# Kernel tuning notes

Hardware: AMD Instinct MI355X
Metric: run time of the kernel (lower is better)

## Reference

```python
import jax, jax.numpy as jnp
import numpy as np

B, T, D = 2, 2048, 1024
H, HD = 16, 64
MAX_LEN = 2048


def setup_inputs() -> dict:
    key = jax.random.key(0)
    ks = jax.random.split(key, 7)
    s = 0.02
    return {
        "x": jax.random.normal(ks[0], (B, T, D), dtype=jnp.float32),
        "qkv_w": jax.random.normal(ks[1], (3 * D, D), dtype=jnp.float32) * s,
        "qkv_b": jax.random.normal(ks[2], (3 * D,), dtype=jnp.float32) * s,
        "out_w": jax.random.normal(ks[3], (D, D), dtype=jnp.float32) * s,
        "out_b": jax.random.normal(ks[4], (D,), dtype=jnp.float32) * s,
        "rel_pos": jax.random.normal(ks[5], (2 * MAX_LEN - 1, HD), dtype=jnp.float32),
        "rpe_w": jax.random.normal(ks[6], (HD,), dtype=jnp.float32) * s,
    }


def reference(x, qkv_w, qkv_b, out_w, out_b, rel_pos, rpe_w):
    Bq, Tq, Dq = x.shape
    scale = HD ** -0.5
    qkv = x @ qkv_w.T + qkv_b  # [B,T,3D]
    qkv = qkv.reshape(Bq, Tq, 3, H, HD)
    q = qkv[:, :, 0].transpose(0, 2, 1, 3)  # [B,H,T,HD]
    k = qkv[:, :, 1].transpose(0, 2, 1, 3)
    v = qkv[:, :, 2].transpose(0, 2, 1, 3)
    scores = jnp.einsum('bhqd,bhkd->bhqk', q, k) * scale  # [B,H,T,T]
    # relative position bias: gather rel embeddings, project to scalar
    rel_idx = jnp.arange(Tq)[None, :] - jnp.arange(Tq)[:, None] + MAX_LEN - 1  # [T,T]
    bias = (rel_pos @ rpe_w)[rel_idx]  # project first (cheap), then gather -> [T,T]
    scores = scores + bias[None, None]
    attn = jax.nn.softmax(scores, axis=-1)
    out = jnp.einsum('bhqk,bhkd->bhqd', attn, v)  # [B,H,T,HD]
    out = out.transpose(0, 2, 1, 3).reshape(Bq, Tq, Dq)
    return out @ out_w.T + out_b
```

## Files before the change

kernel.cpp:

```cpp
#include <hip/hip_runtime.h>
#include <math.h>

#define B_ 2
#define T_ 2048
#define D_ 1024
#define H_ 16
#define HD_ 64
#define MAXLEN_ 2048
#define N3D_ 3072
#define M_ (B_ * T_)
#define KA 1024

#define SCALE_L2E 0.18033688011116215f
#define L2E 1.4426950408889634f

typedef unsigned short ushort_t;
typedef __attribute__((ext_vector_type(8))) short short8;
typedef __attribute__((ext_vector_type(4))) float floatx4;
#define MFMA16(a, b, c) __builtin_amdgcn_mfma_f32_16x16x32_bf16(a, b, c, 0, 0, 0)

static __device__ __forceinline__ ushort_t f2bf(float f) {
    unsigned u = __float_as_uint(f);
    unsigned r = (u + 0x7FFFu + ((u >> 16) & 1u)) >> 16;
    return (ushort_t)r;
}
static __device__ __forceinline__ unsigned packrnu(float a, float b) {
    unsigned ua = __float_as_uint(a) + 0x8000u;
    unsigned ub = __float_as_uint(b) + 0x8000u;
    return __builtin_amdgcn_perm(ub, ua, 0x07060302u);
}

static __device__ __forceinline__ void gld16(const ushort_t* g, ushort_t* l) {
    __builtin_amdgcn_global_load_lds(
        (const __attribute__((address_space(1))) void*)g,
        (__attribute__((address_space(3))) void*)l, 16, 0, 0);
}

__global__ __launch_bounds__(256) void cvt_all(
    const float* __restrict__ x, const float* __restrict__ qw,
    const float* __restrict__ ow, const float* __restrict__ rel_pos,
    const float* __restrict__ rpe_w,
    ushort_t* __restrict__ Xc, ushort_t* __restrict__ QWc,
    ushort_t* __restrict__ OWc, float* __restrict__ biasp)
{
    const int row = blockIdx.x;
    if (row < M_ + N3D_ + D_) {
        const float* src; ushort_t* dst; int r;
        if (row < M_)            { src = x;  dst = Xc;  r = row; }
        else if (row < M_ + N3D_){ src = qw; dst = QWc; r = row - M_; }
        else                     { src = ow; dst = OWc; r = row - M_ - N3D_; }
        const int c = threadIdx.x * 4;
        float4 v = *(const float4*)(src + (size_t)r * 1024 + c);
        ushort4 hv;
        hv.x = f2bf(v.x); hv.y = f2bf(v.y); hv.z = f2bf(v.z); hv.w = f2bf(v.w);
        *(ushort4*)(dst + (size_t)r * KA + c) = hv;
    } else {
        const int wv = threadIdx.x >> 6, lane = threadIdx.x & 63;
        const int r = (row - (M_ + N3D_ + D_)) * 4 + wv;
        if (r < 2 * MAXLEN_ - 1) {
            float v = rel_pos[(size_t)r * HD_ + lane] * rpe_w[lane];
#pragma unroll
            for (int off = 32; off; off >>= 1) v += __shfl_down(v, off);
            if (lane == 0) biasp[r] = v * L2E;
        }
    }
}

__global__ __launch_bounds__(512, 2) void qkv_mfma(
    const ushort_t* __restrict__ Ac, const ushort_t* __restrict__ Bc,
    const float* __restrict__ bias,
    ushort_t* __restrict__ Qs, ushort_t* __restrict__ Khi,
    ushort_t* __restrict__ Vt)
{
    __shared__ __align__(16) ushort_t LDS[2][2][32 * 512];

    const int tid = threadIdx.x;
    const int wv = tid >> 6, lane = tid & 63;
    const int l16 = lane & 15, quad = lane >> 4;
    const int wr = wv >> 2, wc = wv & 3;

    const int orig = blockIdx.y * 12 + blockIdx.x;
    const int swz = (orig & 7) * 24 + (orig >> 3);
    const int m0 = (swz / 12) * 256, n0 = (swz % 12) * 256;

    floatx4 acc[8][4];
#pragma unroll
    for (int i = 0; i < 8; ++i)
#pragma unroll
        for (int j = 0; j < 4; ++j) acc[i][j] = (floatx4){0.f, 0.f, 0.f, 0.f};

    short8 af[4][2];
    short8 bf[2][2][2];

#define BARX() asm volatile("s_barrier" ::: "memory")
#define WAITVM(n) asm volatile("s_waitcnt vmcnt(" #n ")" ::: "memory")

#define STAGE(bufi, ab, unit, tile) do {                                      \
    const ushort_t* _src = (ab) ? Bc : Ac;                                    \
    const int _rc = (ab) ? n0 : m0;                                           \
    const int _I = (unit) * 8 + wv;                                           \
    const ushort_t* _g = _src + (size_t)(_rc + _I * 16 + l16) * KA            \
                              + ((tile) * 64 + quad * 8);                     \
    ushort_t* _l = &LDS[bufi][ab][(_I * 2) * 512];                            \
    gld16(_g, _l);                                                            \
    gld16(_g + 32, _l + 512);                                                 \
} while (0)

#define RD_AF(bufi, mi) do {                                                  \
    _Pragma("unroll") for (int ii = 0; ii < 4; ++ii) {                        \
        const int _I = wr * 8 + (mi) * 4 + ii;                                \
        af[ii][0] = *(const short8*)(&LDS[bufi][0][(_I * 2 + 0) * 512] + lane * 8); \
        af[ii][1] = *(const short8*)(&LDS[bufi][0][(_I * 2 + 1) * 512] + lane * 8); \
    } } while (0)

#define RD_BF(bufi, ni) do {                                                  \
    _Pragma("unroll") for (int jj = 0; jj < 2; ++jj) {                        \
        const int _I = wc * 4 + (ni) * 2 + jj;                                \
        bf[ni][jj][0] = *(const short8*)(&LDS[bufi][1][(_I * 2 + 0) * 512] + lane * 8); \
        bf[ni][jj][1] = *(const short8*)(&LDS[bufi][1][(_I * 2 + 1) * 512] + lane * 8); \
    } } while (0)

#define MM(mi, ni) do {                                                       \
    __builtin_amdgcn_s_setprio(1);                                            \
    _Pragma("unroll") for (int ii = 0; ii < 4; ++ii)                          \
    _Pragma("unroll") for (int jj = 0; jj < 2; ++jj) {                        \
        acc[(mi)*4+ii][(ni)*2+jj] = MFMA16(af[ii][0], bf[ni][jj][0], acc[(mi)*4+ii][(ni)*2+jj]); \
        acc[(mi)*4+ii][(ni)*2+jj] = MFMA16(af[ii][1], bf[ni][jj][1], acc[(mi)*4+ii][(ni)*2+jj]); \
    }                                                                         \
    __builtin_amdgcn_s_setprio(0);                                            \
} while (0)

    STAGE(0, 1, 0, 0); STAGE(0, 1, 1, 0);
    STAGE(0, 0, 0, 0); STAGE(0, 0, 1, 0);
    STAGE(1, 1, 0, 1); STAGE(1, 1, 1, 1);
    WAITVM(4);
    BARX();

#pragma unroll 1
    for (int j = 0; j < 8; ++j) {
        const int tY  = 2 * j + 1;
        const int tX2 = (2 * j + 2) & 15;
        const int tY2 = (2 * j + 3) & 15;
        RD_AF(0, 0); RD_BF(0, 0); STAGE(1, 0, 0, tY);  BARX(); MM(0, 0); BARX();
        RD_BF(0, 1);              STAGE(1, 0, 1, tY);  BARX(); MM(0, 1); BARX();
        RD_AF(0, 1);              STAGE(0, 1, 0, tX2); BARX(); MM(1, 0); BARX();
                                  STAGE(0, 1, 1, tX2); BARX(); MM(1, 1);
        WAITVM(4); BARX();
        RD_AF(1, 0); RD_BF(1, 0); STAGE(0, 0, 0, tX2); BARX(); MM(0, 0); BARX();
        RD_BF(1, 1);              STAGE(0, 0, 1, tX2); BARX(); MM(0, 1); BARX();
        RD_AF(1, 1);              STAGE(1, 1, 0, tY2); BARX(); MM(1, 0); BARX();
                                  STAGE(1, 1, 1, tY2); BARX(); MM(1, 1);
        WAITVM(4); BARX();
    }

#undef BARX
#undef WAITVM
#undef STAGE
#undef RD_AF
#undef RD_BF
#undef MM

#pragma unroll
    for (int mi = 0; mi < 8; ++mi) {
#pragma unroll
        for (int r = 0; r < 4; ++r) {
            const int m = m0 + wr * 128 + mi * 16 + quad * 4 + r;
            const int bb = m >> 11, t = m & 2047;
#pragma unroll
            for (int jj = 0; jj < 4; ++jj) {
                const int n = n0 + wc * 64 + jj * 16 + l16;
                const int c = n >> 10, h = (n >> 6) & 15, hd = n & 63;
                const float v = acc[mi][jj][r] + bias[n];
                const size_t idx = (((size_t)bb * H_ + h) * T_ + t) * HD_ + hd;
                if (c == 0) { Qs[idx] = f2bf(v * SCALE_L2E); }
                else if (c == 1) { Khi[idx] = f2bf(v); }
                else { Vt[(((size_t)bb * H_ + h) * HD_ + hd) * T_ + t] = f2bf(v); }
            }
        }
    }
}

__global__ __launch_bounds__(256) void out_mfma(
    const ushort_t* __restrict__ Ac, const ushort_t* __restrict__ Bc,
    const float* __restrict__ bias, float* __restrict__ Out)
{
    __shared__ __align__(16) ushort_t As[2][16 * 512];
    __shared__ __align__(16) ushort_t Bs[2][8 * 512];
    const int tid = threadIdx.x;
    const int wv = tid >> 6, lane = tid & 63;
    const int l16 = lane & 15, quad = lane >> 4;
    const int wm = wv & 1, wn = wv >> 1;

    const int orig = blockIdx.y * 16 + blockIdx.x;
    const int swz = (orig & 7) * 64 + (orig >> 3);
    const int m0 = (swz >> 4) * 128, n0 = (swz & 15) * 64;

    floatx4 acc[4][2];
#pragma unroll
    for (int i = 0; i < 4; ++i)
#pragma unroll
        for (int j = 0; j < 2; ++j) acc[i][j] = (floatx4){0.f, 0.f, 0.f, 0.f};

    auto stage = [&](int bufi, int kk) {
#pragma unroll
        for (int c = 0; c < 4; ++c) {
            const int b = wv * 4 + c;
            const int i = b >> 1, ks = b & 1;
            const int k = kk + ks * 32 + quad * 8;
            gld16(Ac + (size_t)(m0 + i * 16 + l16) * KA + k, As[bufi] + b * 512);
        }
#pragma unroll
        for (int c = 0; c < 2; ++c) {
            const int b = wv * 2 + c;
            const int j = b >> 1, ks = b & 1;
            const int k = kk + ks * 32 + quad * 8;
            gld16(Bc + (size_t)(n0 + j * 16 + l16) * KA + k, Bs[bufi] + b * 512);
        }
    };

    stage(0, 0);
    __syncthreads();

#pragma unroll 1
    for (int t = 0; t < 16; ++t) {
        const int cur = t & 1;
        if (t < 15) stage(cur ^ 1, (t + 1) * 64);
#pragma unroll
        for (int ks = 0; ks < 2; ++ks) {
            short8 af[4], bf[2];
#pragma unroll
            for (int ii = 0; ii < 4; ++ii)
                af[ii] = *(const short8*)(As[cur] + ((wm * 4 + ii) * 2 + ks) * 512 + lane * 8);
#pragma unroll
            for (int jj = 0; jj < 2; ++jj)
                bf[jj] = *(const short8*)(Bs[cur] + ((wn * 2 + jj) * 2 + ks) * 512 + lane * 8);
#pragma unroll
            for (int ii = 0; ii < 4; ++ii)
#pragma unroll
                for (int jj = 0; jj < 2; ++jj)
                    acc[ii][jj] = MFMA16(af[ii], bf[jj], acc[ii][jj]);
        }
        if (t < 15) __syncthreads();
    }

#pragma unroll
    for (int ii = 0; ii < 4; ++ii) {
#pragma unroll
        for (int r = 0; r < 4; ++r) {
            const int m = m0 + wm * 64 + ii * 16 + quad * 4 + r;
#pragma unroll
            for (int jj = 0; jj < 2; ++jj) {
                const int n = n0 + wn * 32 + jj * 16 + l16;
                Out[(size_t)m * D_ + n] = acc[ii][jj][r] + bias[n];
            }
        }
    }
}

__global__ __launch_bounds__(256) void attn_mfma(
    const ushort_t* __restrict__ Qs, const ushort_t* __restrict__ Khi,
    const ushort_t* __restrict__ Vt, const float* __restrict__ biasp,
    ushort_t* __restrict__ AOc)
{
    __shared__ __align__(16) ushort_t KS[2][8 * 512];
    __shared__ __align__(16) ushort_t VS[2][8 * 512];
    __shared__ __align__(16) ushort_t PS[4][2][1024];

    const int i = blockIdx.x;
    const int j = i >> 3;
    const int bh = (i & 7) + 8 * (j >> 4);
    const int q0 = (j & 15) * 128;
    const int tid = threadIdx.x;
    const int wv = tid >> 6, lane = tid & 63;
    const int l16 = lane & 15, quad = lane >> 4;

    const int qw = q0 + wv * 32;

    short8 qh[2][2];
#pragma unroll
    for (int u = 0; u < 2; ++u) {
        const size_t qoff = ((size_t)bh * T_ + qw + u * 16 + l16) * HD_ + quad * 8;
        qh[u][0] = *(const short8*)(Qs + qoff);
        qh[u][1] = *(const short8*)(Qs + qoff + 32);
    }

    float l_r[2] = {0.f, 0.f};
    floatx4 o_acc[4][2];
#pragma unroll
    for (int g2 = 0; g2 < 4; ++g2)
#pragma unroll
        for (int u = 0; u < 2; ++u) o_acc[g2][u] = (floatx4){0.f, 0.f, 0.f, 0.f};

    const ushort_t* gK = Khi + (size_t)bh * T_ * HD_;
    const ushort_t* gV = Vt + (size_t)bh * HD_ * T_;
    const int c0base = 2047 + quad * 4 - (qw + 16 + l16);
    const int qdbase = quad >> 1;

    const size_t kstage = (size_t)(wv * 16 + l16) * HD_ + quad * 8;
    const size_t vstage = (size_t)(wv * 16 + l16) * T_ + quad * 8;

    gld16(gK + kstage,      KS[0] + (wv * 2 + 0) * 512);
    gld16(gK + kstage + 32, KS[0] + (wv * 2 + 1) * 512);
    gld16(gV + vstage,      VS[0] + (wv * 2 + 0) * 512);
    gld16(gV + vstage + 32, VS[0] + (wv * 2 + 1) * 512);
    __syncthreads();

    for (int t = 0; t < 32; ++t) {
        const int k0 = t * 64;
        const int buf = t & 1, nbuf = buf ^ 1;

        float4 f4[5];
        {
            const float* bp = biasp + (c0base + k0);
#pragma unroll
            for (int z = 0; z < 5; ++z)
                __builtin_memcpy(&f4[z], bp + z * 16, 16);
        }

        if (t < 31) {
            const size_t koff = kstage + (size_t)(k0 + 64) * HD_;
            gld16(gK + koff,      KS[nbuf] + (wv * 2 + 0) * 512);
            gld16(gK + koff + 32, KS[nbuf] + (wv * 2 + 1) * 512);
            const size_t voff = vstage + (size_t)(k0 + 64);
            gld16(gV + voff,      VS[nbuf] + (wv * 2 + 0) * 512);
            gld16(gV + voff + 32, VS[nbuf] + (wv * 2 + 1) * 512);
        }

#pragma unroll
        for (int g = 0; g < 4; ++g) {
            const short8 kh0 = *(const short8*)(KS[buf] + (g * 2 + 0) * 512 + lane * 8);
            const short8 kh1 = *(const short8*)(KS[buf] + (g * 2 + 1) * 512 + lane * 8);
            const int qd = 2 * (g & 1) + qdbase;
#pragma unroll
            for (int u = 0; u < 2; ++u) {
                const float4 bbv = f4[g + 1 - u];
                floatx4 a = (floatx4){bbv.x, bbv.y, bbv.z, bbv.w};
                a = MFMA16(kh0, qh[u][0], a);
                a = MFMA16(kh1, qh[u][1], a);
                const float p0 = __builtin_amdgcn_exp2f(a[0]);
                const float p1 = __builtin_amdgcn_exp2f(a[1]);
                const float p2 = __builtin_amdgcn_exp2f(a[2]);
                const float p3 = __builtin_amdgcn_exp2f(a[3]);
                l_r[u] += (p0 + p1) + (p2 + p3);
                uint2 pkd;
                pkd.x = packrnu(p0, p1);
                pkd.y = packrnu(p2, p3);
                *(uint2*)(PS[wv][u] + (g >> 1) * 512 + (qd * 16 + l16) * 8 + (quad & 1) * 4) = pkd;
            }
        }

        short8 pf[2][2];
#pragma unroll
        for (int u = 0; u < 2; ++u) {
            pf[u][0] = *(const short8*)(PS[wv][u] + lane * 8);
            pf[u][1] = *(const short8*)(PS[wv][u] + 512 + lane * 8);
        }

#pragma unroll
        for (int g2 = 0; g2 < 4; ++g2) {
            const short8 v0 = *(const short8*)(VS[buf] + (g2 * 2 + 0) * 512 + lane * 8);
            const short8 v1 = *(const short8*)(VS[buf] + (g2 * 2 + 1) * 512 + lane * 8);
#pragma unroll
            for (int u = 0; u < 2; ++u) {
                o_acc[g2][u] = MFMA16(v0, pf[u][0], o_acc[g2][u]);
                o_acc[g2][u] = MFMA16(v1, pf[u][1], o_acc[g2][u]);
            }
        }
        __syncthreads();
    }

    const int bb2 = bh >> 4, h2 = bh & 15;
#pragma unroll
    for (int u = 0; u < 2; ++u) {
        l_r[u] += __shfl_xor(l_r[u], 16);
        l_r[u] += __shfl_xor(l_r[u], 32);
        const float inv = 1.0f / l_r[u];
        const size_t m = (size_t)bb2 * T_ + qw + u * 16 + l16;
#pragma unroll
        for (int g2 = 0; g2 < 4; ++g2) {
            uint2 pk;
            pk.x = packrnu(o_acc[g2][u][0] * inv, o_acc[g2][u][1] * inv);
            pk.y = packrnu(o_acc[g2][u][2] * inv, o_acc[g2][u][3] * inv);
            *(uint2*)(AOc + m * KA + h2 * 64 + g2 * 16 + quad * 4) = pk;
        }
    }
}

extern "C" void kernel_launch(void* const* d_in, const int* in_sizes, int n_in,
                              void* d_out, int out_size, void* d_ws, size_t ws_size,
                              hipStream_t stream)
{
    const float* x       = (const float*)d_in[0];
    const float* qkv_w   = (const float*)d_in[1];
    const float* qkv_b   = (const float*)d_in[2];
    const float* out_w   = (const float*)d_in[3];
    const float* out_b   = (const float*)d_in[4];
    const float* rel_pos = (const float*)d_in[5];
    const float* rpe_w   = (const float*)d_in[6];
    float* out = (float*)d_out;

    const size_t QE = (size_t)B_ * H_ * T_ * HD_;
    ushort_t* Qs  = (ushort_t*)d_ws;
    ushort_t* Khi = Qs  + QE;
    ushort_t* Vt  = Khi + QE;
    ushort_t* Xc  = Vt  + QE;
    ushort_t* QWc = Xc  + (size_t)M_ * KA;
    ushort_t* OWc = QWc + (size_t)N3D_ * KA;
    ushort_t* AOc = OWc + (size_t)D_ * KA;
    float* biasp  = (float*)(AOc + (size_t)M_ * KA);

    cvt_all<<<M_ + N3D_ + D_ + 1024, 256, 0, stream>>>(
        x, qkv_w, out_w, rel_pos, rpe_w, Xc, QWc, OWc, biasp);

    qkv_mfma<<<dim3(12, 16), 512, 0, stream>>>(
        Xc, QWc, qkv_b, Qs, Khi, Vt);
    attn_mfma<<<512, 256, 0, stream>>>(Qs, Khi, Vt, biasp, AOc);
    out_mfma<<<dim3(D_ / 64, M_ / 128), 256, 0, stream>>>(
        AOc, OWc, out_b, out);
}
```

Baseline: 241.9 us.

## Halve attention query tile per block and swizzle P staging in LDS

Each attention block now handles 64 queries (16 per wave) instead of 128, doubling the grid to 1024 blocks and setting launch bounds to 4 blocks per SM. The shared P buffer is cut to one tile per wave and its addresses are XOR-swizzled to reduce LDS bank conflicts. The intent is more parallelism and occupancy across the 256 CUs. The cost is that each K/V tile loaded into LDS now feeds half as many queries, doubling K/V traffic per unit of work.

```diff
diff --git a/kernel.cpp b/kernel.cpp
--- a/kernel.cpp
+++ b/kernel.cpp
@@ -257,44 +257,40 @@
     }
 }
 
-__global__ __launch_bounds__(256) void attn_mfma(
+__global__ __launch_bounds__(256, 4) void attn_mfma(
     const ushort_t* __restrict__ Qs, const ushort_t* __restrict__ Khi,
     const ushort_t* __restrict__ Vt, const float* __restrict__ biasp,
     ushort_t* __restrict__ AOc)
 {
     __shared__ __align__(16) ushort_t KS[2][8 * 512];
     __shared__ __align__(16) ushort_t VS[2][8 * 512];
-    __shared__ __align__(16) ushort_t PS[4][2][1024];
+    __shared__ __align__(16) ushort_t PS[4][1024];
 
     const int i = blockIdx.x;
     const int j = i >> 3;
-    const int bh = (i & 7) + 8 * (j >> 4);
-    const int q0 = (j & 15) * 128;
+    const int bh = (i & 7) + 8 * (j >> 5);
+    const int q0 = (j & 31) * 64;
     const int tid = threadIdx.x;
     const int wv = tid >> 6, lane = tid & 63;
     const int l16 = lane & 15, quad = lane >> 4;
 
-    const int qw = q0 + wv * 32;
-
-    short8 qh[2][2];
-#pragma unroll
-    for (int u = 0; u < 2; ++u) {
-        const size_t qoff = ((size_t)bh * T_ + qw + u * 16 + l16) * HD_ + quad * 8;
-        qh[u][0] = *(const short8*)(Qs + qoff);
-        qh[u][1] = *(const short8*)(Qs + qoff + 32);
-    }
-
-    float l_r[2] = {0.f, 0.f};
-    floatx4 o_acc[4][2];
-#pragma unroll
-    for (int g2 = 0; g2 < 4; ++g2)
-#pragma unroll
-        for (int u = 0; u < 2; ++u) o_acc[g2][u] = (floatx4){0.f, 0.f, 0.f, 0.f};
+    const int qw = q0 + wv * 16;
+
+    short8 qh[2];
+    {
+        const size_t qoff = ((size_t)bh * T_ + qw + l16) * HD_ + quad * 8;
+        qh[0] = *(const short8*)(Qs + qoff);
+        qh[1] = *(const short8*)(Qs + qoff + 32);
+    }
+
+    float l_r = 0.f;
+    floatx4 o_acc[4];
+#pragma unroll
+    for (int g2 = 0; g2 < 4; ++g2) o_acc[g2] = (floatx4){0.f, 0.f, 0.f, 0.f};
 
     const ushort_t* gK = Khi + (size_t)bh * T_ * HD_;
     const ushort_t* gV = Vt + (size_t)bh * HD_ * T_;
-    const int c0base = 2047 + quad * 4 - (qw + 16 + l16);
-    const int qdbase = quad >> 1;
+    const int c0base = 2047 + quad * 4 - (qw + l16);
 
     const size_t kstage = (size_t)(wv * 16 + l16) * HD_ + quad * 8;
     const size_t vstage = (size_t)(wv * 16 + l16) * T_ + quad * 8;
@@ -305,15 +301,17 @@
     gld16(gV + vstage + 32, VS[0] + (wv * 2 + 1) * 512);
     __syncthreads();
 
+#define PSW(u) ((u) ^ ((((u) >> 6) & 3) << 4))
+
     for (int t = 0; t < 32; ++t) {
         const int k0 = t * 64;
         const int buf = t & 1, nbuf = buf ^ 1;
 
-        float4 f4[5];
+        float4 f4[4];
         {
             const float* bp = biasp + (c0base + k0);
 #pragma unroll
-            for (int z = 0; z < 5; ++z)
+            for (int z = 0; z < 4; ++z)
                 __builtin_memcpy(&f4[z], bp + z * 16, 16);
         }
 
@@ -330,59 +328,53 @@
         for (int g = 0; g < 4; ++g) {
             const short8 kh0 = *(const short8*)(KS[buf] + (g * 2 + 0) * 512 + lane * 8);
             const short8 kh1 = *(const short8*)(KS[buf] + (g * 2 + 1) * 512 + lane * 8);
-            const int qd = 2 * (g & 1) + qdbase;
-#pragma unroll
-            for (int u = 0; u < 2; ++u) {
-                const float4 bbv = f4[g + 1 - u];
-                floatx4 a = (floatx4){bbv.x, bbv.y, bbv.z, bbv.w};
-                a = MFMA16(kh0, qh[u][0], a);
-                a = MFMA16(kh1, qh[u][1], a);
-                const float p0 = __builtin_amdgcn_exp2f(a[0]);
-                const float p1 = __builtin_amdgcn_exp2f(a[1]);
-                const float p2 = __builtin_amdgcn_exp2f(a[2]);
-                const float p3 = __builtin_amdgcn_exp2f(a[3]);
-                l_r[u] += (p0 + p1) + (p2 + p3);
-                uint2 pkd;
-                pkd.x = packrnu(p0, p1);
-                pkd.y = packrnu(p2, p3);
-                *(uint2*)(PS[wv][u] + (g >> 1) * 512 + (qd * 16 + l16) * 8 + (quad & 1) * 4) = pkd;
-            }
-        }
-
-        short8 pf[2][2];
-#pragma unroll
-        for (int u = 0; u < 2; ++u) {
-            pf[u][0] = *(const short8*)(PS[wv][u] + lane * 8);
-            pf[u][1] = *(const short8*)(PS[wv][u] + 512 + lane * 8);
+            const float4 bbv = f4[g];
+            floatx4 a = (floatx4){bbv.x, bbv.y, bbv.z, bbv.w};
+            a = MFMA16(kh0, qh[0], a);
+            a = MFMA16(kh1, qh[1], a);
+            const float p0 = __builtin_amdgcn_exp2f(a[0]);
+            const float p1 = __builtin_amdgcn_exp2f(a[1]);
+            const float p2 = __builtin_amdgcn_exp2f(a[2]);
+            const float p3 = __builtin_amdgcn_exp2f(a[3]);
+            l_r += (p0 + p1) + (p2 + p3);
+            uint2 pkd;
+            pkd.x = packrnu(p0, p1);
+            pkd.y = packrnu(p2, p3);
+            const int qd = 2 * (g & 1) + (quad >> 1);
+            const int widx = (g >> 1) * 512 + (qd * 16 + l16) * 8 + (quad & 1) * 4;
+            *(uint2*)(PS[wv] + PSW(widx)) = pkd;
+        }
+
+        short8 pf[2];
+        {
+            const int r0 = lane * 8, r1 = 512 + lane * 8;
+            pf[0] = *(const short8*)(PS[wv] + PSW(r0));
+            pf[1] = *(const short8*)(PS[wv] + PSW(r1));
         }
 
 #pragma unroll
         for (int g2 = 0; g2 < 4; ++g2) {
             const short8 v0 = *(const short8*)(VS[buf] + (g2 * 2 + 0) * 512 + lane * 8);
             const short8 v1 = *(const short8*)(VS[buf] + (g2 * 2 + 1) * 512 + lane * 8);
-#pragma unroll
-            for (int u = 0; u < 2; ++u) {
-                o_acc[g2][u] = MFMA16(v0, pf[u][0], o_acc[g2][u]);
-                o_acc[g2][u] = MFMA16(v1, pf[u][1], o_acc[g2][u]);
-            }
+            o_acc[g2] = MFMA16(v0, pf[0], o_acc[g2]);
+            o_acc[g2] = MFMA16(v1, pf[1], o_acc[g2]);
         }
         __syncthreads();
     }
 
+#undef PSW
+
     const int bb2 = bh >> 4, h2 = bh & 15;
-#pragma unroll
-    for (int u = 0; u < 2; ++u) {
-        l_r[u] += __shfl_xor(l_r[u], 16);
-        l_r[u] += __shfl_xor(l_r[u], 32);
-        const float inv = 1.0f / l_r[u];
-        const size_t m = (size_t)bb2 * T_ + qw + u * 16 + l16;
-#pragma unroll
-        for (int g2 = 0; g2 < 4; ++g2) {
-            uint2 pk;
-            pk.x = packrnu(o_acc[g2][u][0] * inv, o_acc[g2][u][1] * inv);
-            pk.y = packrnu(o_acc[g2][u][2] * inv, o_acc[g2][u][3] * inv);
-            *(uint2*)(AOc + m * KA + h2 * 64 + g2 * 16 + quad * 4) = pk;
-        }
+    l_r += __shfl_xor(l_r, 16);
+    l_r += __shfl_xor(l_r, 32);
+    const float inv = 1.0f / l_r;
+    const size_t m = (size_t)bb2 * T_ + qw + l16;
+#pragma unroll
+    for (int g2 = 0; g2 < 4; ++g2) {
+        uint2 pk;
+        pk.x = packrnu(o_acc[g2][0] * inv, o_acc[g2][1] * inv);
+        pk.y = packrnu(o_acc[g2][2] * inv, o_acc[g2][3] * inv);
+        *(uint2*)(AOc + m * KA + h2 * 64 + g2 * 16 + quad * 4) = pk;
     }
 }
 
@@ -414,7 +406,7 @@
 
     qkv_mfma<<<dim3(12, 16), 512, 0, stream>>>(
         Xc, QWc, qkv_b, Qs, Khi, Vt);
-    attn_mfma<<<512, 256, 0, stream>>>(Qs, Khi, Vt, biasp, AOc);
+    attn_mfma<<<1024, 256, 0, stream>>>(Qs, Khi, Vt, biasp, AOc);
     out_mfma<<<dim3(D_ / 64, M_ / 128), 256, 0, stream>>>(
         AOc, OWc, out_b, out);
 }
```

Measured after the change: 255.7 us. 5.7% more time.
